# Optimization experiments

Measured on AMD Instinct MI355X. Metric: run time of the kernel, lower is better.

## Reference

```python
import jax, jax.numpy as jnp
import numpy as np

EPS_MSG = 1e-7
EPS_BN = 1e-5


def _seg_softmax(logits, seg, num_segments):
    # logits: [E, D] per-edge logits; softmax over edges sharing the same dst node
    m = jax.ops.segment_max(logits, seg, num_segments=num_segments)
    m = jnp.where(jnp.isfinite(m), m, 0.0)
    e = jnp.exp(logits - m[seg])
    s = jax.ops.segment_sum(e, seg, num_segments=num_segments)
    return e / (s[seg] + 1e-16)


def _batchnorm(h, gamma, beta):
    mu = jnp.mean(h, axis=0)
    var = jnp.var(h, axis=0)
    return (h - mu) * jax.lax.rsqrt(var + EPS_BN) * gamma + beta


def setup_inputs() -> dict:
    key = jax.random.key(0)
    ks = jax.random.split(key, 12)
    N, E, G, D, L = 100000, 600000, 512, 128, 7
    x = jax.random.randint(ks[0], (N, 9), 0, 64, dtype=jnp.int32)
    edge_index = jax.random.randint(ks[1], (2, E), 0, N, dtype=jnp.int32)
    edge_attr = jax.random.randint(ks[2], (E, 3), 0, 8, dtype=jnp.int32)
    batch = jnp.sort(jax.random.randint(ks[3], (N,), 0, G, dtype=jnp.int32))
    rf_pred = jax.random.uniform(ks[4], (G,), dtype=jnp.float32)
    atom_emb = jax.random.normal(ks[5], (9, 64, D), dtype=jnp.float32) * 0.02
    bond_emb = jax.random.normal(ks[6], (3, 8, D), dtype=jnp.float32) * 0.02
    conv_w = jax.random.normal(ks[7], (L, D, D), dtype=jnp.float32) * 0.02
    conv_b = jnp.zeros((L, D), dtype=jnp.float32)
    ts = jnp.ones((L,), dtype=jnp.float32)  # learnable inverse temperatures (init 1/t style)
    gammas = jnp.ones((L, D), dtype=jnp.float32)
    bn_betas = jnp.zeros((L, D), dtype=jnp.float32)
    final_w = jax.random.normal(ks[8], (D, 1), dtype=jnp.float32) * 0.02
    final_b = jnp.zeros((1,), dtype=jnp.float32)
    beta = jnp.array([0.5], dtype=jnp.float32)
    return {"x": x, "edge_index": edge_index, "edge_attr": edge_attr, "batch": batch,
            "rf_pred": rf_pred, "atom_emb": atom_emb, "bond_emb": bond_emb,
            "conv_w": conv_w, "conv_b": conv_b, "ts": ts, "gammas": gammas,
            "bn_betas": bn_betas, "final_w": final_w, "final_b": final_b, "beta": beta}


def reference(x, edge_index, edge_attr, batch, rf_pred, atom_emb, bond_emb,
              conv_w, conv_b, ts, gammas, bn_betas, final_w, final_b, beta):
    N = x.shape[0]
    G = rf_pred.shape[0]
    L = conv_w.shape[0]
    src, dst = edge_index[0], edge_index[1]

    # AtomEncoder / BondEncoder: sum of per-feature embeddings
    h = jax.vmap(lambda tab, idx: tab[idx], in_axes=(0, 1))(atom_emb, x).sum(0)          # [N, D]
    e_emb = jax.vmap(lambda tab, idx: tab[idx], in_axes=(0, 1))(bond_emb, edge_attr).sum(0)  # [E, D]

    def genconv(l, hin):
        msg = jax.nn.relu(hin[src] + e_emb) + EPS_MSG          # [E, D]
        alpha = _seg_softmax(msg * ts[l], dst, N)              # softmax aggregation weights
        aggr = jax.ops.segment_sum(alpha * msg, dst, num_segments=N)  # [N, D]
        return (hin + aggr) @ conv_w[l] + conv_b[l]

    # res+ DeeperGCN
    h = genconv(0, h)
    for l in range(1, L):
        h2 = jax.nn.relu(_batchnorm(h, gammas[l - 1], bn_betas[l - 1]))
        h = genconv(l, h2) + h
    h = jax.nn.relu(_batchnorm(h, gammas[L - 1], bn_betas[L - 1]))

    # mean graph pooling
    counts = jnp.maximum(jax.ops.segment_sum(jnp.ones((N,), h.dtype), batch, num_segments=G), 1.0)
    hg = jax.ops.segment_sum(h, batch, num_segments=G) / counts[:, None]  # [G, D]

    dgcn_pred = hg @ final_w + final_b  # [G, 1]
    return (1.0 - beta) * jax.nn.sigmoid(dgcn_pred) + beta * rf_pred.reshape(-1, 1)
```

## Files before the change

### kernel.cpp

```cpp
#include <hip/hip_runtime.h>
#include <hip/hip_fp16.h>
#include <math.h>

#define D 128
#define PF 12

typedef _Float16 f16x8 __attribute__((ext_vector_type(8)));
typedef _Float16 f16x2 __attribute__((ext_vector_type(2)));
typedef float f32x4_t __attribute__((ext_vector_type(4)));

static __device__ __forceinline__ f16x2 h2v(__half2 h) {
    union { __half2 h; f16x2 v; } u; u.h = h; return u.v;
}
static __device__ __forceinline__ __half2 v2h(f16x2 v) {
    union { f16x2 v; __half2 h; } u; u.v = v; return u.h;
}


__global__ void hist_kernel(const int* __restrict__ edge_index, int* __restrict__ deg, int E) {
    int e = blockIdx.x * blockDim.x + threadIdx.x;
    if (e >= E) return;
    atomicAdd(&deg[edge_index[E + e]], 1);
}

__global__ void scanA_kernel(const int* __restrict__ deg, int* __restrict__ bsum, int n) {
    __shared__ int red[256];
    int b = blockIdx.x, t = threadIdx.x;
    int base = b * 1024 + t * 4;
    int s = 0;
#pragma unroll
    for (int j = 0; j < 4; ++j)
        if (base + j < n) s += deg[base + j];
    red[t] = s;
    __syncthreads();
    for (int off = 128; off > 0; off >>= 1) {
        if (t < off) red[t] += red[t + off];
        __syncthreads();
    }
    if (t == 0) bsum[b] = red[0];
}

__global__ void scanC_kernel(const int* __restrict__ deg, const int* __restrict__ bsum,
                             int nb, int* __restrict__ row_start, int* __restrict__ cursor,
                             int n) {
    __shared__ int sh[256];
    __shared__ int sb[256];
    int b = blockIdx.x, t = threadIdx.x;
    sb[t] = (t < nb) ? bsum[t] : 0;
    int base = b * 1024 + t * 4;
    int v[4];
#pragma unroll
    for (int j = 0; j < 4; ++j) v[j] = (base + j < n) ? deg[base + j] : 0;
    int p[4];
    p[0] = 0; p[1] = v[0]; p[2] = v[0] + v[1]; p[3] = v[0] + v[1] + v[2];
    int s = p[3] + v[3];
    sh[t] = s;
    __syncthreads();
    for (int off = 1; off < 256; off <<= 1) {
        int x = (t >= off) ? sh[t - off] : 0;
        int y = (t >= off) ? sb[t - off] : 0;
        __syncthreads();
        sh[t] += x;
        sb[t] += y;
        __syncthreads();
    }
    int boffb = (b == 0) ? 0 : sb[b - 1];
    int off0 = boffb + sh[t] - s;
#pragma unroll
    for (int j = 0; j < 4; ++j)
        if (base + j < n) {
            row_start[base + j] = off0 + p[j];
            cursor[base + j] = off0 + p[j];
        }
    if (base <= n - 1 && n - 1 < base + 4) row_start[n] = off0 + s;
}

__global__ void scatter_misc_kernel(const int* __restrict__ edge_index,
                                    const int* __restrict__ edge_attr,
                                    int* __restrict__ cursor, int2* __restrict__ csr, int E,
                                    const int* __restrict__ x, const float* __restrict__ atom_emb,
                                    _Float16* __restrict__ h16, int ndTotal,
                                    const float* __restrict__ bond_emb, __half2* __restrict__ evt,
                                    const float* __restrict__ conv_w, _Float16* __restrict__ wt,
                                    int wtTotal, const int* __restrict__ batch,
                                    int* __restrict__ gstart, int N, int G) {
    int idx = blockIdx.x * blockDim.x + threadIdx.x;
    if (idx < E) {
        int src = edge_index[idx];
        int dst = edge_index[E + idx];
        int pos = atomicAdd(&cursor[dst], 1);
        int a0 = edge_attr[idx * 3], a1 = edge_attr[idx * 3 + 1], a2 = edge_attr[idx * 3 + 2];
        csr[pos] = make_int2(src, a0 | (a1 << 3) | (a2 << 6));
        return;
    }
    idx -= E;
    if (idx < ndTotal) {
        int n = idx >> 7;
        int d = idx & 127;
        float acc = 0.f;
#pragma unroll
        for (int f = 0; f < 9; ++f) {
            int v = x[n * 9 + f];
            acc += atom_emb[(long long)(f * 64 + v) * D + d];
        }
        h16[idx] = (_Float16)acc;
        return;
    }
    idx -= ndTotal;
    if (idx < 512 * 64) {
        int combo = idx >> 6, j = idx & 63;
        int d0 = 2 * j;
        float ex = bond_emb[(combo & 7) * D + d0] +
                   bond_emb[(8 + ((combo >> 3) & 7)) * D + d0] +
                   bond_emb[(16 + ((combo >> 6) & 7)) * D + d0];
        float ey = bond_emb[(combo & 7) * D + d0 + 1] +
                   bond_emb[(8 + ((combo >> 3) & 7)) * D + d0 + 1] +
                   bond_emb[(16 + ((combo >> 6) & 7)) * D + d0 + 1];
        evt[idx] = __floats2half2_rn(ex, ey);
        return;
    }
    int widx = idx - 512 * 64;
    if (widx < wtTotal) {
        int l = widx >> 14;
        int rem = widx & 16383;
        int n = rem >> 7, k = rem & 127;
        wt[widx] = (_Float16)conv_w[(l << 14) + k * 128 + n];
        return;
    }
    int n = widx - wtTotal;
    if (n >= N) return;
    if (n == 0) {
        for (int g = 0; g <= batch[0]; ++g) gstart[g] = 0;
    } else {
        int b0 = batch[n - 1], b1 = batch[n];
        for (int g = b0 + 1; g <= b1; ++g) gstart[g] = n;
    }
    if (n == N - 1) {
        for (int g = batch[N - 1] + 1; g <= G; ++g) gstart[g] = N;
    }
}


__global__ void bn_finalize_kernel(const float* __restrict__ acc4,
                                   const float* __restrict__ gamma,
                                   const float* __restrict__ bnbeta, float invN,
                                   float* __restrict__ aArr, float* __restrict__ bArr) {
    int t = threadIdx.x;
    float s1 = acc4[t] + acc4[256 + t] + acc4[512 + t] + acc4[768 + t];
    float s2 = acc4[128 + t] + acc4[384 + t] + acc4[640 + t] + acc4[896 + t];
    float mean = s1 * invN;
    float var = s2 * invN - mean * mean;
    float a = rsqrtf(var + 1e-5f) * gamma[t];
    aArr[t] = a;
    bArr[t] = bnbeta[t] - mean * a;
}

__global__ __launch_bounds__(128, 8) void fused_layer_kernel(
        const __half2* __restrict__ h16c,
        const float* __restrict__ aArr, const float* __restrict__ bArr, int applyBN,
        const float* __restrict__ ts, int l,
        const int* __restrict__ row_start, const int2* __restrict__ csr,
        const __half2* __restrict__ evt,
        const _Float16* __restrict__ wt, const float* __restrict__ bias,
        int residual, _Float16* __restrict__ h16out,
        float* __restrict__ accL, int N) {
    __shared__ __align__(16) char smem[8192];
    _Float16* yh = (_Float16*)smem;
    __half2* tile2 = (__half2*)smem;

    int t = threadIdx.x;
    int row0 = blockIdx.x * 16;
    int wave = t >> 6;
    int lane = t & 63;
    float tsl = ts[l];
    int a = row0 + wave * 8;

    f16x2 zerov = (f16x2)(_Float16)0;
    f16x2 bnA2 = zerov, bnB2 = zerov;
    if (applyBN) {
        float2 af = ((const float2*)aArr)[lane];
        float2 bf = ((const float2*)bArr)[lane];
        bnA2[0] = (_Float16)af.x; bnA2[1] = (_Float16)af.y;
        bnB2[0] = (_Float16)bf.x; bnB2[1] = (_Float16)bf.y;
    }
    __half2 zero2 = v2h(zerov);

    int rsv = row_start[min(a + min(lane, 8), N)];
    __half2 hsv0 = zero2, hsv1 = zero2, hsv2 = zero2, hsv3 = zero2;
    __half2 hsv4 = zero2, hsv5 = zero2, hsv6 = zero2, hsv7 = zero2;
    if (a + 0 < N) hsv0 = h16c[(size_t)(a + 0) * 64 + lane];
    if (a + 1 < N) hsv1 = h16c[(size_t)(a + 1) * 64 + lane];
    if (a + 2 < N) hsv2 = h16c[(size_t)(a + 2) * 64 + lane];
    if (a + 3 < N) hsv3 = h16c[(size_t)(a + 3) * 64 + lane];
    if (a + 4 < N) hsv4 = h16c[(size_t)(a + 4) * 64 + lane];
    if (a + 5 < N) hsv5 = h16c[(size_t)(a + 5) * 64 + lane];
    if (a + 6 < N) hsv6 = h16c[(size_t)(a + 6) * 64 + lane];
    if (a + 7 < N) hsv7 = h16c[(size_t)(a + 7) * 64 + lane];

    int s0 = __builtin_amdgcn_readlane(rsv, 0);
    int s1 = __builtin_amdgcn_readlane(rsv, 8);

    int c0 = s0;
    int2 eaCur = make_int2(0, 0), eaNxt = make_int2(0, 0);
    if (c0 + lane < s1) eaCur = csr[c0 + lane];
    if (c0 + 64 + lane < s1) eaNxt = csr[c0 + 64 + lane];

    __half2 hvS[PF], evS[PF];
#pragma unroll
    for (int k = 0; k < PF; ++k) {
        int pp = s0 + k;
        if (pp < s1) {
            int srcp = __builtin_amdgcn_readlane(eaCur.x, k);
            int cbp = __builtin_amdgcn_readlane(eaCur.y, k);
            hvS[k] = h16c[(size_t)srcp * 64 + lane];
            evS[k] = evt[(size_t)cbp * 64 + lane];
        }
    }

    float accwx = 0.f, accwy = 0.f, accmx = 0.f, accmy = 0.f;
    int cur = 0;
    int nend = __builtin_amdgcn_readlane(rsv, 1);

#define CLOSE_ROW()                                                           \
    {                                                                         \
        __half2 hh;                                                           \
        switch (cur) {                                                        \
            case 0: hh = hsv0; break; case 1: hh = hsv1; break;               \
            case 2: hh = hsv2; break; case 3: hh = hsv3; break;               \
            case 4: hh = hsv4; break; case 5: hh = hsv5; break;               \
            case 6: hh = hsv6; break; default: hh = hsv7; break;              \
        }                                                                     \
        f16x2 hvv = h2v(hh);                                                  \
        if (applyBN)                                                          \
            hvv = __builtin_elementwise_max(hvv * bnA2 + bnB2, zerov);        \
        float2 yy;                                                            \
        yy.x = (float)hvv[0] + __fdividef(accmx, accwx + 1e-16f) + 1e-7f;     \
        yy.y = (float)hvv[1] + __fdividef(accmy, accwy + 1e-16f) + 1e-7f;     \
        tile2[(wave * 8 + cur) * 68 + lane] = __floats2half2_rn(yy.x, yy.y);  \
        accwx = accwy = accmx = accmy = 0.f;                                  \
        cur++;                                                                \
        nend = __builtin_amdgcn_readlane(rsv, min(cur + 1, 8));               \
    }

    while (cur < 8 && nend == s0) CLOSE_ROW();

    int total = s1 - s0;
    for (int it = 0; it < total; it += PF) {
#pragma unroll
        for (int k = 0; k < PF; ++k) {
            int p = s0 + it + k;
            if (p < s1) {
                f16x2 hv2 = h2v(hvS[k]);
                if (applyBN)
                    hv2 = __builtin_elementwise_max(hv2 * bnA2 + bnB2, zerov);
                f16x2 m2 = __builtin_elementwise_max(hv2 + h2v(evS[k]), zerov);
                float mx = (float)m2[0];
                float my = (float)m2[1];
                float wx = __expf(mx * tsl);
                float wy = __expf(my * tsl);
                accwx += wx; accmx = fmaf(wx, mx, accmx);
                accwy += wy; accmy = fmaf(wy, my, accmy);
                int pp = p + PF;
                if (pp < s1) {
                    if (pp >= c0 + 64) {
                        c0 += 64;
                        eaCur = eaNxt;
                        eaNxt = make_int2(0, 0);
                        if (c0 + 64 + lane < s1) eaNxt = csr[c0 + 64 + lane];
                    }
                    int q = pp - c0;
                    int srcp = __builtin_amdgcn_readlane(eaCur.x, q);
                    int cbp = __builtin_amdgcn_readlane(eaCur.y, q);
                    hvS[k] = h16c[(size_t)srcp * 64 + lane];
                    evS[k] = evt[(size_t)cbp * 64 + lane];
                }
                while (cur < 8 && nend == p + 1) CLOSE_ROW();
            }
        }
    }
#undef CLOSE_ROW
    __syncthreads();

    int ln = t & 15;
    int quad = (t & 63) >> 4;
    const _Float16* h16in = (const _Float16*)h16c;

    float cs[4] = {0.f, 0.f, 0.f, 0.f};
    float cq[4] = {0.f, 0.f, 0.f, 0.f};
    const _Float16* ap = yh + ln * 136 + quad * 8;
#pragma unroll
    for (int ct = 0; ct < 4; ++ct) {
        int colg = (wave * 4 + ct) * 16 + ln;
        const _Float16* bp = wt + (size_t)colg * 128 + quad * 8;
        f32x4_t c = {0.f, 0.f, 0.f, 0.f};
#pragma unroll
        for (int kk = 0; kk < 4; ++kk) {
            f16x8 av = *(const f16x8*)(ap + kk * 32);
            f16x8 bv = *(const f16x8*)(bp + kk * 32);
            c = __builtin_amdgcn_mfma_f32_16x16x32_f16(av, bv, c, 0, 0, 0);
        }
        float bsv = bias[colg];
#pragma unroll
        for (int reg = 0; reg < 4; ++reg) {
            int r = row0 + quad * 4 + reg;
            if (r < N) {
                long long off = (long long)r * D + colg;
                float o = c[reg] + bsv;
                if (residual) o += (float)h16in[off];
                h16out[off] = (_Float16)o;
                cs[ct] += o; cq[ct] += o * o;
            }
        }
    }

    __syncthreads();
    float* stats = (float*)smem;
    int grp = wave * 4 + quad;
#pragma unroll
    for (int ct = 0; ct < 4; ++ct) {
        int colg = (wave * 4 + ct) * 16 + ln;
        stats[grp * 256 + colg] = cs[ct];
        stats[grp * 256 + 128 + colg] = cq[ct];
    }
    __syncthreads();
    float ssumA = 0.f, ssumB = 0.f;
#pragma unroll
    for (int g = 0; g < 8; ++g) {
        ssumA += stats[g * 256 + t];
        ssumB += stats[g * 256 + 128 + t];
    }
    int cbase = (blockIdx.x & 3) << 8;
    atomicAdd(&accL[cbase + t], ssumA);
    atomicAdd(&accL[cbase + 128 + t], ssumB);
}

__global__ void pool_head_kernel(const __half2* __restrict__ h16,
                                 const float* __restrict__ acc4,
                                 const float* __restrict__ gamma,
                                 const float* __restrict__ bnbeta, float invN,
                                 const int* __restrict__ gstart,
                                 const float* __restrict__ fw, const float* __restrict__ fb,
                                 const float* __restrict__ beta, const float* __restrict__ rf,
                                 float* __restrict__ out) {
    __shared__ float redx[256], redy[256];
    __shared__ float sA[128], sB[128];
    int g = blockIdx.x, t = threadIdx.x;
    if (t < 128) {
        float s1 = acc4[t] + acc4[256 + t] + acc4[512 + t] + acc4[768 + t];
        float s2 = acc4[128 + t] + acc4[384 + t] + acc4[640 + t] + acc4[896 + t];
        float mean = s1 * invN;
        float var = s2 * invN - mean * mean;
        float a = rsqrtf(var + 1e-5f) * gamma[t];
        sA[t] = a;
        sB[t] = bnbeta[t] - mean * a;
    }
    __syncthreads();
    int d2 = t & 63, sub = t >> 6;
    int s0 = gstart[g], s1 = gstart[g + 1];
    float2 a2 = make_float2(sA[2 * d2], sA[2 * d2 + 1]);
    float2 b2 = make_float2(sB[2 * d2], sB[2 * d2 + 1]);
    float ax = 0.f, ay = 0.f;
    for (int n = s0 + sub; n < s1; n += 4) {
        f16x2 v = h2v(h16[(size_t)n * 64 + d2]);
        ax += fmaxf((float)v[0] * a2.x + b2.x, 0.f);
        ay += fmaxf((float)v[1] * a2.y + b2.y, 0.f);
    }
    redx[t] = ax; redy[t] = ay;
    __syncthreads();
    if (t < 64) {
        float sx = redx[t] + redx[t + 64] + redx[t + 128] + redx[t + 192];
        float sy = redy[t] + redy[t + 64] + redy[t + 128] + redy[t + 192];
        float v = sx * fw[2 * t] + sy * fw[2 * t + 1];
#pragma unroll
        for (int off = 32; off > 0; off >>= 1) v += __shfl_down(v, off);
        if (t == 0) {
            float c = fmaxf((float)(s1 - s0), 1.f);
            float pred = v / c + fb[0];
            float sig = 1.f / (1.f + __expf(-pred));
            float bb = beta[0];
            out[g] = (1.f - bb) * sig + bb * rf[g];
        }
    }
}

static inline size_t align16(size_t x) { return (x + 15) & ~(size_t)15; }

extern "C" void kernel_launch(void* const* d_in, const int* in_sizes, int n_in,
                              void* d_out, int out_size, void* d_ws, size_t ws_size,
                              hipStream_t stream) {
    const int* x = (const int*)d_in[0];
    const int* edge_index = (const int*)d_in[1];
    const int* edge_attr = (const int*)d_in[2];
    const int* batch = (const int*)d_in[3];
    const float* rf_pred = (const float*)d_in[4];
    const float* atom_emb = (const float*)d_in[5];
    const float* bond_emb = (const float*)d_in[6];
    const float* conv_w = (const float*)d_in[7];
    const float* conv_b = (const float*)d_in[8];
    const float* ts = (const float*)d_in[9];
    const float* gammas = (const float*)d_in[10];
    const float* bn_betas = (const float*)d_in[11];
    const float* final_w = (const float*)d_in[12];
    const float* final_b = (const float*)d_in[13];
    const float* beta = (const float*)d_in[14];
    float* out = (float*)d_out;

    int N = in_sizes[0] / 9;
    int E = in_sizes[1] / 2;
    int G = in_sizes[4];
    int L = in_sizes[9];

    int nTiles = (N + 15) / 16;
    size_t ND = (size_t)N * D;
    size_t accFloats = (size_t)L * 1024;

    char* p = (char*)d_ws;
    _Float16* h16_a = (_Float16*)p;  p += align16(ND * 2);
    _Float16* h16_b = (_Float16*)p;  p += align16(ND * 2);
    __half2* evt = (__half2*)p;      p += align16((size_t)512 * 64 * 4);
    _Float16* wt = (_Float16*)p;     p += align16((size_t)L * 16384 * 2);
    float* aArr = (float*)p;         p += align16((size_t)D * 4);
    float* bArr = (float*)p;         p += align16((size_t)D * 4);
    int* gstart = (int*)p;           p += align16((size_t)(G + 1) * 4);
    float* acc = (float*)p;          p += align16(accFloats * 4);
    int* deg = (int*)p;              p += align16((size_t)N * 4);
    int* row_start = (int*)p;        p += align16((size_t)(N + 1) * 4);
    int* cursor = (int*)p;           p += align16((size_t)N * 4);
    int* bsum = (int*)p;             p += align16((size_t)256 * 4);
    int2* csr = (int2*)p;            p += align16((size_t)E * 8);

    int eBlocks = (E + 255) / 256;
    int nb1024 = (N + 1023) / 1024;
    int wtTotal = L * 16384;
    int ndTotal = N * D;
    int smTotal = E + ndTotal + 512 * 64 + wtTotal + N;
    int smBlocks = (smTotal + 255) / 256;
    float invN = 1.0f / (float)N;

    (void)hipMemsetAsync(acc, 0, align16(accFloats * 4) + (size_t)N * 4, stream);
    hist_kernel<<<eBlocks, 256, 0, stream>>>(edge_index, deg, E);
    scanA_kernel<<<nb1024, 256, 0, stream>>>(deg, bsum, N);
    scanC_kernel<<<nb1024, 256, 0, stream>>>(deg, bsum, nb1024, row_start, cursor, N);
    scatter_misc_kernel<<<smBlocks, 256, 0, stream>>>(edge_index, edge_attr, cursor, csr, E,
                                                      x, atom_emb, h16_a, ndTotal,
                                                      bond_emb, evt, conv_w, wt, wtTotal,
                                                      batch, gstart, N, G);

    _Float16* h16c = h16_a;
    _Float16* h16n = h16_b;
    for (int l = 0; l < L; ++l) {
        int applyBN = (l >= 1) ? 1 : 0;
        if (applyBN) {
            bn_finalize_kernel<<<1, 128, 0, stream>>>(
                acc + (size_t)(l - 1) * 1024, gammas + (size_t)(l - 1) * D,
                bn_betas + (size_t)(l - 1) * D, invN, aArr, bArr);
        }
        fused_layer_kernel<<<nTiles, 128, 0, stream>>>(
            (const __half2*)h16c, aArr, bArr, applyBN, ts, l, row_start, csr, evt,
            wt + (size_t)l * 16384, conv_b + (size_t)l * D,
            applyBN, h16n, acc + (size_t)l * 1024, N);
        _Float16* tmp16 = h16c; h16c = h16n; h16n = tmp16;
    }

    pool_head_kernel<<<G, 256, 0, stream>>>(
        (const __half2*)h16c, acc + (size_t)(L - 1) * 1024,
        gammas + (size_t)(L - 1) * D, bn_betas + (size_t)(L - 1) * D, invN,
        gstart, final_w, final_b, beta, rf_pred, out);
}
```

Before: 847.7 us.

## Replace per-block BN stat atomics with partial buffer and separate reduction kernel

Each tile block now writes its column sum and sum-of-squares to a per-block partial buffer instead of issuing global atomics into four shared copies. A new 256-block reduction kernel folds these partials into the accumulator after each layer. The BN finalize kernel is removed: every fused layer block recomputes the scale and shift from the accumulator itself. This aims to cut atomic contention in the hot kernel at the cost of an extra launch per layer and about 50 MB of partial-buffer traffic.

```diff
diff --git a/kernel.cpp b/kernel.cpp
--- a/kernel.cpp
+++ b/kernel.cpp
@@ -141,29 +141,25 @@
 }
 
 
-__global__ void bn_finalize_kernel(const float* __restrict__ acc4,
-                                   const float* __restrict__ gamma,
-                                   const float* __restrict__ bnbeta, float invN,
-                                   float* __restrict__ aArr, float* __restrict__ bArr) {
-    int t = threadIdx.x;
-    float s1 = acc4[t] + acc4[256 + t] + acc4[512 + t] + acc4[768 + t];
-    float s2 = acc4[128 + t] + acc4[384 + t] + acc4[640 + t] + acc4[896 + t];
-    float mean = s1 * invN;
-    float var = s2 * invN - mean * mean;
-    float a = rsqrtf(var + 1e-5f) * gamma[t];
-    aArr[t] = a;
-    bArr[t] = bnbeta[t] - mean * a;
+__global__ void bn_stage1_kernel(const float* __restrict__ partial, int nb,
+                                 float* __restrict__ acc4) {
+    int b = blockIdx.x, t = threadIdx.x;
+    float s = 0.f;
+    for (int r = b; r < nb; r += 256)
+        s += partial[(long long)r * 256 + t];
+    atomicAdd(&acc4[((b & 3) << 8) + t], s);
 }
 
 __global__ __launch_bounds__(128, 8) void fused_layer_kernel(
         const __half2* __restrict__ h16c,
-        const float* __restrict__ aArr, const float* __restrict__ bArr, int applyBN,
+        const float* __restrict__ accPrev, const float* __restrict__ gammaPrev,
+        const float* __restrict__ betaPrev, float invN, int applyBN,
         const float* __restrict__ ts, int l,
         const int* __restrict__ row_start, const int2* __restrict__ csr,
         const __half2* __restrict__ evt,
         const _Float16* __restrict__ wt, const float* __restrict__ bias,
         int residual, _Float16* __restrict__ h16out,
-        float* __restrict__ accL, int N) {
+        float* __restrict__ partial, int N) {
     __shared__ __align__(16) char smem[8192];
     _Float16* yh = (_Float16*)smem;
     __half2* tile2 = (__half2*)smem;
@@ -176,13 +172,6 @@
     int a = row0 + wave * 8;
 
     f16x2 zerov = (f16x2)(_Float16)0;
-    f16x2 bnA2 = zerov, bnB2 = zerov;
-    if (applyBN) {
-        float2 af = ((const float2*)aArr)[lane];
-        float2 bf = ((const float2*)bArr)[lane];
-        bnA2[0] = (_Float16)af.x; bnA2[1] = (_Float16)af.y;
-        bnB2[0] = (_Float16)bf.x; bnB2[1] = (_Float16)bf.y;
-    }
     __half2 zero2 = v2h(zerov);
 
     int rsv = row_start[min(a + min(lane, 8), N)];
@@ -196,6 +185,27 @@
     if (a + 5 < N) hsv5 = h16c[(size_t)(a + 5) * 64 + lane];
     if (a + 6 < N) hsv6 = h16c[(size_t)(a + 6) * 64 + lane];
     if (a + 7 < N) hsv7 = h16c[(size_t)(a + 7) * 64 + lane];
+
+    f16x2 bnA2 = zerov, bnB2 = zerov;
+    if (applyBN) {
+        float s1x = 0.f, s1y = 0.f, s2x = 0.f, s2y = 0.f;
+#pragma unroll
+        for (int c = 0; c < 4; ++c) {
+            float2 u = ((const float2*)(accPrev + c * 256))[lane];
+            float2 v = ((const float2*)(accPrev + c * 256 + 128))[lane];
+            s1x += u.x; s1y += u.y; s2x += v.x; s2y += v.y;
+        }
+        float2 gm = ((const float2*)gammaPrev)[lane];
+        float2 bb = ((const float2*)betaPrev)[lane];
+        float meanx = s1x * invN, meany = s1y * invN;
+        float varx = s2x * invN - meanx * meanx;
+        float vary = s2y * invN - meany * meany;
+        float ax = rsqrtf(varx + 1e-5f) * gm.x;
+        float ay = rsqrtf(vary + 1e-5f) * gm.y;
+        bnA2[0] = (_Float16)ax; bnA2[1] = (_Float16)ay;
+        bnB2[0] = (_Float16)(bb.x - meanx * ax);
+        bnB2[1] = (_Float16)(bb.y - meany * ay);
+    }
 
     int s0 = __builtin_amdgcn_readlane(rsv, 0);
     int s1 = __builtin_amdgcn_readlane(rsv, 8);
@@ -329,9 +339,8 @@
         ssumA += stats[g * 256 + t];
         ssumB += stats[g * 256 + 128 + t];
     }
-    int cbase = (blockIdx.x & 3) << 8;
-    atomicAdd(&accL[cbase + t], ssumA);
-    atomicAdd(&accL[cbase + 128 + t], ssumB);
+    partial[(long long)blockIdx.x * 256 + t] = ssumA;
+    partial[(long long)blockIdx.x * 256 + 128 + t] = ssumB;
 }
 
 __global__ void pool_head_kernel(const __half2* __restrict__ h16,
@@ -419,8 +428,7 @@
     _Float16* h16_b = (_Float16*)p;  p += align16(ND * 2);
     __half2* evt = (__half2*)p;      p += align16((size_t)512 * 64 * 4);
     _Float16* wt = (_Float16*)p;     p += align16((size_t)L * 16384 * 2);
-    float* aArr = (float*)p;         p += align16((size_t)D * 4);
-    float* bArr = (float*)p;         p += align16((size_t)D * 4);
+    float* partial = (float*)p;      p += align16((size_t)256 * nTiles * 4);
     int* gstart = (int*)p;           p += align16((size_t)(G + 1) * 4);
     float* acc = (float*)p;          p += align16(accFloats * 4);
     int* deg = (int*)p;              p += align16((size_t)N * 4);
@@ -450,15 +458,15 @@
     _Float16* h16n = h16_b;
     for (int l = 0; l < L; ++l) {
         int applyBN = (l >= 1) ? 1 : 0;
-        if (applyBN) {
-            bn_finalize_kernel<<<1, 128, 0, stream>>>(
-                acc + (size_t)(l - 1) * 1024, gammas + (size_t)(l - 1) * D,
-                bn_betas + (size_t)(l - 1) * D, invN, aArr, bArr);
-        }
+        const float* accPrev = (l >= 1) ? (acc + (size_t)(l - 1) * 1024) : acc;
+        const float* gmPrev = (l >= 1) ? (gammas + (size_t)(l - 1) * D) : gammas;
+        const float* bbPrev = (l >= 1) ? (bn_betas + (size_t)(l - 1) * D) : bn_betas;
         fused_layer_kernel<<<nTiles, 128, 0, stream>>>(
-            (const __half2*)h16c, aArr, bArr, applyBN, ts, l, row_start, csr, evt,
-            wt + (size_t)l * 16384, conv_b + (size_t)l * D,
-            applyBN, h16n, acc + (size_t)l * 1024, N);
+            (const __half2*)h16c, accPrev, gmPrev, bbPrev, invN, applyBN, ts, l,
+            row_start, csr, evt, wt + (size_t)l * 16384, conv_b + (size_t)l * D,
+            applyBN, h16n, partial, N);
+        bn_stage1_kernel<<<256, 256, 0, stream>>>(partial, nTiles,
+                                                  acc + (size_t)l * 1024);
         _Float16* tmp16 = h16c; h16c = h16n; h16n = tmp16;
     }
 
```

Result: faster. 772.5 us (-8.9%).
